# Performance work log

Hardware: AMD Instinct MI355X
Metric: run time of the kernel (lower is better)

## Reference

```python
import jax, jax.numpy as jnp
import numpy as np

HEADS = 16
DHEAD = 128
B, S, DMODEL = 2, 2048, 2048


def setup_inputs() -> dict:
    key = jax.random.key(0)
    k1, k2, k3 = jax.random.split(key, 3)
    x = jax.random.normal(k1, (B, S, DMODEL), dtype=jnp.float32)
    # Linear weights, stored as [in, out] so forward is x @ w (no bias).
    w_in = jax.random.normal(k2, (DMODEL, 3 * HEADS * DHEAD), dtype=jnp.float32) * (DMODEL ** -0.5)
    w_out = jax.random.normal(k3, (HEADS * DHEAD, DMODEL), dtype=jnp.float32) * ((HEADS * DHEAD) ** -0.5)
    # Causal mask: True = masked (strictly upper triangular), broadcast over batch & heads.
    mask = jnp.triu(jnp.ones((S, S), dtype=jnp.bool_), k=1)[None, None, :, :]
    return {"x": x, "w_in": w_in, "w_out": w_out, "mask": mask}


def reference(x, w_in, w_out, mask):
    b, s, _ = x.shape
    # Fused QKV projection: [b,s,3*H*dh] -> [b,s,H,3*dh] -> chunk into q,k,v [b,s,H,dh]
    projected = (x @ w_in).reshape(b, s, HEADS, 3 * DHEAD)
    q, k, v = jnp.split(projected, 3, axis=-1)
    # Scores [b,H,l,L], scaled by 1/sqrt(dhead)
    scale = 1.0 / (DHEAD ** 0.5)
    a = jnp.einsum("blhd,bLhd->bhlL", q, k) * scale
    a = jnp.where(mask, -jnp.inf, a)
    a = jax.nn.softmax(a, axis=-1)
    # Weighted values -> [b,l,H,dh] -> flatten heads -> output projection
    out = jnp.einsum("bhlL,bLhd->blhd", a, v).reshape(b, s, HEADS * DHEAD)
    return out @ w_out
```

## Files before the change

### kernel.cpp

```cpp
#include <hip/hip_runtime.h>

#define HD    16
#define DH    128
#define BB    2
#define SS    2048
#define DM    2048
#define NQKV  6144
#define MTOT  4096

typedef short   bfx8  __attribute__((ext_vector_type(8)));
typedef float   f32x4 __attribute__((ext_vector_type(4)));

__device__ __forceinline__ unsigned short f2bf(float f) {
  union { float f; unsigned int u; } c; c.f = f;
  unsigned int u = c.u + 0x7FFFu + ((c.u >> 16) & 1u);
  return (unsigned short)(u >> 16);
}

__device__ __forceinline__ void gload_lds16(const unsigned short* g, unsigned short* l) {
  __builtin_amdgcn_global_load_lds(
      (const __attribute__((address_space(1))) unsigned int*)g,
      (__attribute__((address_space(3))) unsigned int*)l, 16, 0, 0);
}

#define BARS() do { asm volatile("s_waitcnt lgkmcnt(0)" ::: "memory");               \
                    __builtin_amdgcn_sched_barrier(0); __builtin_amdgcn_s_barrier(); \
                    __builtin_amdgcn_sched_barrier(0); } while (0)
#define VMCNT10() do { asm volatile("s_waitcnt vmcnt(10)" ::: "memory"); \
                       __builtin_amdgcn_sched_barrier(0); } while (0)
#define VMCNT6() do { asm volatile("s_waitcnt vmcnt(6)" ::: "memory"); \
                      __builtin_amdgcn_sched_barrier(0); } while (0)

__global__ __launch_bounds__(256) void prep_fused_k(const float* __restrict__ x,
                                                    unsigned short* __restrict__ Xb,
                                                    const float* __restrict__ w_in,
                                                    unsigned short* __restrict__ Wit) {
  __shared__ float t[32][33];
  const int bid = (int)blockIdx.x;
  if (bid < 8192) {
    const int i = bid * 256 + (int)threadIdx.x;
    const float4 v = *(const float4*)(x + (size_t)i * 4);
    ushort4 o;
    o.x = f2bf(v.x); o.y = f2bf(v.y); o.z = f2bf(v.z); o.w = f2bf(v.w);
    *(ushort4*)(Xb + (size_t)i * 4) = o;
    return;
  }
  const int tb = bid - 8192;
  const int c0 = (tb % 192) * 32, r0 = (tb / 192) * 32;
  const int tx = threadIdx.x & 31, ty = threadIdx.x >> 5;
#pragma unroll
  for (int i = 0; i < 4; i++) {
    int r = r0 + ty + i * 8;
    t[ty + i * 8][tx] = w_in[(size_t)r * NQKV + c0 + tx];
  }
  __syncthreads();
#pragma unroll
  for (int i = 0; i < 4; i++) {
    int c = c0 + ty + i * 8;
    Wit[(size_t)c * DM + r0 + tx] = f2bf(t[tx][ty + i * 8]);
  }
}

__global__ __launch_bounds__(256, 2) void gemm128_qkv_k(const unsigned short* __restrict__ A,
                                                        const unsigned short* __restrict__ Bt,
                                                        unsigned short* __restrict__ Qg,
                                                        unsigned short* __restrict__ Kg,
                                                        unsigned short* __restrict__ Vg,
                                                        int K) {
  __shared__ __align__(16) unsigned short Asb[2][128 * 64];
  __shared__ __align__(16) unsigned short Bsb[2][192 * 64];
  const int tid = threadIdx.x;
  const int lane = tid & 63, wid = tid >> 6;
  const int wr = wid >> 1, wc = wid & 1;
  const int cbase = lane & 15, rgrp = lane >> 4;
  const int bid = (int)blockIdx.x;
  const int id = (bid & 7) * 128 + (bid >> 3);
  const int nb = id >> 5, mb = id & 31;
  const size_t m0 = (size_t)mb * 128, n0 = (size_t)nb * 192;
  const int nkt = K >> 6;

#define STAGE_A32(u_, g_) do {                                                          \
    const int uc_ = ((u_) < nkt ? (u_) : (nkt - 1));                                    \
    const int r_ = tid >> 3, s_ = tid & 7;                                              \
    gload_lds16(A + (m0 + (g_) * 32 + r_) * (size_t)K + uc_ * 64 +                      \
                    (((s_ * 16) ^ ((r_ & 7) << 4)) >> 1),                               \
                &Asb[(u_) & 1][(g_) * 2048] + tid * 8); } while (0)
#define STAGE_B32(u_, g_) do {                                                          \
    const int uc_ = ((u_) < nkt ? (u_) : (nkt - 1));                                    \
    const int r_ = tid >> 3, s_ = tid & 7;                                              \
    gload_lds16(Bt + (n0 + (g_) * 32 + r_) * (size_t)K + uc_ * 64 +                     \
                    (((s_ * 16) ^ ((r_ & 7) << 4)) >> 1),                               \
                &Bsb[(u_) & 1][(g_) * 2048] + tid * 8); } while (0)

  const int axor = (cbase & 7) << 4;
  int a_off[2], b_off[2];
#pragma unroll
  for (int ks = 0; ks < 2; ks++) {
    a_off[ks] = ((wr * 64 + cbase) * 128 + ((ks * 64 + rgrp * 16) ^ axor)) >> 1;
    b_off[ks] = ((wc * 96 + cbase) * 128 + ((ks * 64 + rgrp * 16) ^ axor)) >> 1;
  }

#define RD_AALL(dst_, p_) do { _Pragma("unroll")                                         \
    for (int mf_ = 0; mf_ < 4; mf_++) { _Pragma("unroll")                                \
      for (int ks_ = 0; ks_ < 2; ks_++)                                                  \
        dst_[mf_][ks_] = *(const bfx8*)((p_) + a_off[ks_] + mf_ * 1024); } } while (0)
#define RD_BP(dst_, p_, P_) do { _Pragma("unroll")                                       \
    for (int nf_ = 0; nf_ < 2; nf_++) { _Pragma("unroll")                                \
      for (int ks_ = 0; ks_ < 2; ks_++)                                                  \
        dst_[nf_][ks_] = *(const bfx8*)((p_) + b_off[ks_] + (nf_ + (P_)) * 1024); } } while (0)

#define MFMA_P(no_, AF_, BF_) do {                                                       \
    __builtin_amdgcn_s_setprio(1);                                                      \
    _Pragma("unroll")                                                                    \
    for (int mf_ = 0; mf_ < 4; mf_++) { _Pragma("unroll")                                \
      for (int nf_ = 0; nf_ < 2; nf_++) { _Pragma("unroll")                              \
        for (int ks_ = 0; ks_ < 2; ks_++)                                                \
          acc[mf_][nf_ + (no_)] = __builtin_amdgcn_mfma_f32_16x16x32_bf16(               \
              AF_[mf_][ks_], BF_[nf_][ks_], acc[mf_][nf_ + (no_)], 0, 0, 0); } }         \
    __builtin_amdgcn_s_setprio(0); } while (0)

  f32x4 acc[4][6];
  const f32x4 z = {0.f, 0.f, 0.f, 0.f};
#pragma unroll
  for (int mf = 0; mf < 4; mf++)
#pragma unroll
    for (int nf = 0; nf < 6; nf++) acc[mf][nf] = z;

  STAGE_A32(0, 0); STAGE_A32(0, 1); STAGE_A32(0, 2); STAGE_A32(0, 3);
  STAGE_B32(0, 0); STAGE_B32(0, 1); STAGE_B32(0, 2);
  STAGE_B32(0, 3); STAGE_B32(0, 4); STAGE_B32(0, 5);
  STAGE_A32(1, 0); STAGE_A32(1, 1); STAGE_A32(1, 2); STAGE_A32(1, 3);
  STAGE_B32(1, 0); STAGE_B32(1, 1); STAGE_B32(1, 2);
  STAGE_B32(1, 3); STAGE_B32(1, 4); STAGE_B32(1, 5);
  VMCNT10();
  BARS();
  bfx8 aA[4][2], b01A[2][2], aB[4][2], b01B[2][2];
  RD_AALL(aA, &Asb[0][0]);
  RD_BP(b01A, &Bsb[0][0], 0);
  BARS();

#define TILE_BODY(u_, Ac, B01c, An, B01n) do {                                           \
    const unsigned short* Bs_  = &Bsb[(u_) & 1][0];                                      \
    const unsigned short* Asn_ = &Asb[((u_) + 1) & 1][0];                                \
    const unsigned short* Bsn_ = &Bsb[((u_) + 1) & 1][0];                                \
    bfx8 b23[2][2], b45[2][2];                                                           \
        \
                                                             \
    RD_BP(b23, Bs_, 2);                                                                  \
    STAGE_A32((u_) + 2, 0); STAGE_A32((u_) + 2, 1);                                      \
    STAGE_A32((u_) + 2, 2); STAGE_A32((u_) + 2, 3);                                      \
    STAGE_B32((u_) + 2, 0); STAGE_B32((u_) + 2, 3);                                      \
    BARS();                                                                              \
    MFMA_P(0, Ac, B01c);                                                                 \
         \
    RD_BP(b45, Bs_, 4);                                                                  \
    STAGE_B32((u_) + 2, 1); STAGE_B32((u_) + 2, 4);                                      \
    BARS();                                                                              \
    MFMA_P(2, Ac, b23);                                                                  \
        \
                                           \
    STAGE_B32((u_) + 2, 2); STAGE_B32((u_) + 2, 5);                                      \
    VMCNT10();                                                                           \
    BARS();                                                                              \
    RD_AALL(An, Asn_);                                                                   \
    RD_BP(B01n, Bsn_, 0);                                                                \
    MFMA_P(4, Ac, b45);                                                                  \
    BARS();                                                                              \
  } while (0)

#pragma unroll 1
  for (int u = 0; u < nkt; u += 2) {
    TILE_BODY(u,     aA, b01A, aB, b01B);
    TILE_BODY(u + 1, aB, b01B, aA, b01A);
  }
#undef TILE_BODY
#undef STAGE_A32
#undef STAGE_B32

#pragma unroll
  for (int mf = 0; mf < 4; mf++)
#pragma unroll
    for (int nf = 0; nf < 6; nf++) {
      const int nn = (int)n0 + wc * 96 + nf * 16;
      const int h = nn / 384, tt = (nn >> 7) % 3;
      const int d = (nn & 127) + cbase;
      const int row0 = (int)m0 + wr * 64 + mf * 16 + rgrp * 4;
      const int bb = row0 >> 11;
      const int s0 = row0 & 2047;
      if (tt == 2) {
        ushort4 v;
        v.x = f2bf(acc[mf][nf][0]); v.y = f2bf(acc[mf][nf][1]);
        v.z = f2bf(acc[mf][nf][2]); v.w = f2bf(acc[mf][nf][3]);
        *(ushort4*)(Vg + ((size_t)(bb * HD + h) * DH + d) * SS + s0) = v;
      } else {
        unsigned short* dst = (tt == 0 ? Qg : Kg);
#pragma unroll
        for (int r = 0; r < 4; r++)
          dst[((size_t)(bb * HD + h) * SS + s0 + r) * DH + d] = f2bf(acc[mf][nf][r]);
      }
    }
}

__global__ __launch_bounds__(512, 2) void gemm256_out_k(const unsigned short* __restrict__ A,
                                                        const unsigned short* __restrict__ Bt,
                                                        float* __restrict__ C, int K, int ldc) {
  __shared__ __align__(16) unsigned short Asb[2][256 * 64];
  __shared__ __align__(16) unsigned short Bsb[2][128 * 64];
  const int tid = threadIdx.x;
  const int lane = tid & 63, wid = tid >> 6;
  const int wr = wid >> 2, wc = wid & 3;
  const int cbase = lane & 15, rgrp = lane >> 4;
  const int bid = (int)blockIdx.x;
  const int id = (bid & 7) * 32 + (bid >> 3);
  const int nb = id >> 4, mb = id & 15;
  const size_t m0 = (size_t)mb * 256, n0 = (size_t)nb * 128;
  const int nkt = K >> 6;

#define STAGE_AO(u_, g_) do {                                                           \
    const int uc_ = ((u_) < nkt ? (u_) : (nkt - 1));                                    \
    const int r_ = tid >> 3, s_ = tid & 7;                                              \
    gload_lds16(A + (m0 + (g_) * 64 + r_) * (size_t)K + uc_ * 64 +                      \
                    (((s_ * 16) ^ ((r_ & 7) << 4)) >> 1),                               \
                &Asb[(u_) & 1][(g_) * 4096] + tid * 8); } while (0)
#define STAGE_BO(u_, g_) do {                                                           \
    const int uc_ = ((u_) < nkt ? (u_) : (nkt - 1));                                    \
    const int r_ = tid >> 3, s_ = tid & 7;                                              \
    gload_lds16(Bt + (n0 + (g_) * 64 + r_) * (size_t)K + uc_ * 64 +                     \
                    (((s_ * 16) ^ ((r_ & 7) << 4)) >> 1),                               \
                &Bsb[(u_) & 1][(g_) * 4096] + tid * 8); } while (0)

  const int axor = (cbase & 7) << 4;
  int a_off[2], b_off[2];
#pragma unroll
  for (int ks = 0; ks < 2; ks++) {
    a_off[ks] = ((wr * 128 + cbase) * 128 + ((ks * 64 + rgrp * 16) ^ axor)) >> 1;
    b_off[ks] = ((wc * 32 + cbase) * 128 + ((ks * 64 + rgrp * 16) ^ axor)) >> 1;
  }

#define RD_A03(dst_, p_) do { _Pragma("unroll")                                          \
    for (int mf_ = 0; mf_ < 4; mf_++) { _Pragma("unroll")                                \
      for (int ks_ = 0; ks_ < 2; ks_++)                                                  \
        dst_[mf_][ks_] = *(const bfx8*)((p_) + a_off[ks_] + mf_ * 1024); } } while (0)
#define RD_A47(dst_, p_) do { _Pragma("unroll")                                          \
    for (int mf_ = 0; mf_ < 4; mf_++) { _Pragma("unroll")                                \
      for (int ks_ = 0; ks_ < 2; ks_++)                                                  \
        dst_[mf_][ks_] = *(const bfx8*)((p_) + a_off[ks_] + (mf_ + 4) * 1024); } } while (0)
#define RD_B01(dst_, p_) do { _Pragma("unroll")                                          \
    for (int nf_ = 0; nf_ < 2; nf_++) { _Pragma("unroll")                                \
      for (int ks_ = 0; ks_ < 2; ks_++)                                                  \
        dst_[nf_][ks_] = *(const bfx8*)((p_) + b_off[ks_] + nf_ * 1024); } } while (0)

#define MFMA_O(mo_, AF_, BF_) do {                                                       \
    __builtin_amdgcn_s_setprio(1);                                                      \
    _Pragma("unroll")                                                                    \
    for (int mf_ = 0; mf_ < 4; mf_++) { _Pragma("unroll")                                \
      for (int nf_ = 0; nf_ < 2; nf_++) { _Pragma("unroll")                              \
        for (int ks_ = 0; ks_ < 2; ks_++)                                                \
          acc[mf_ + (mo_)][nf_] = __builtin_amdgcn_mfma_f32_16x16x32_bf16(               \
              AF_[mf_][ks_], BF_[nf_][ks_], acc[mf_ + (mo_)][nf_], 0, 0, 0); } }         \
    __builtin_amdgcn_s_setprio(0); } while (0)

  f32x4 acc[8][2];
  const f32x4 z = {0.f, 0.f, 0.f, 0.f};
#pragma unroll
  for (int mf = 0; mf < 8; mf++)
#pragma unroll
    for (int nf = 0; nf < 2; nf++) acc[mf][nf] = z;

  STAGE_AO(0, 0); STAGE_AO(0, 1); STAGE_AO(0, 2); STAGE_AO(0, 3);
  STAGE_BO(0, 0); STAGE_BO(0, 1);
  STAGE_AO(1, 0); STAGE_AO(1, 1); STAGE_AO(1, 2); STAGE_AO(1, 3);
  STAGE_BO(1, 0); STAGE_BO(1, 1);
  VMCNT6();
  BARS();
  bfx8 a03A[4][2], b01A[2][2], a03B[4][2], b01B[2][2];
  RD_A03(a03A, &Asb[0][0]);
  RD_B01(b01A, &Bsb[0][0]);
  BARS();

#define TILE_BODY_O(u_, A03c, B01c, A03n, B01n) do {                                     \
    const unsigned short* As_  = &Asb[(u_) & 1][0];                                      \
    const unsigned short* Asn_ = &Asb[((u_) + 1) & 1][0];                                \
    const unsigned short* Bsn_ = &Bsb[((u_) + 1) & 1][0];                                \
    bfx8 a47[4][2];                                                                      \
    RD_A47(a47, As_);                                                                    \
    STAGE_AO((u_) + 2, 0); STAGE_AO((u_) + 2, 2);                                        \
    BARS();                                                                              \
    MFMA_O(0, A03c, B01c);                                                               \
    STAGE_AO((u_) + 2, 1); STAGE_AO((u_) + 2, 3);                                        \
    STAGE_BO((u_) + 2, 0); STAGE_BO((u_) + 2, 1);                                        \
    VMCNT6();                                                                            \
    BARS();                                                                              \
    RD_A03(A03n, Asn_);                                                                  \
    RD_B01(B01n, Bsn_);                                                                  \
    MFMA_O(4, a47, B01c);                                                                \
    BARS();                                                                              \
  } while (0)

#pragma unroll 1
  for (int u = 0; u < nkt; u += 2) {
    TILE_BODY_O(u,     a03A, b01A, a03B, b01B);
    TILE_BODY_O(u + 1, a03B, b01B, a03A, b01A);
  }
#undef TILE_BODY_O
#undef STAGE_AO
#undef STAGE_BO

#pragma unroll
  for (int mf = 0; mf < 8; mf++)
#pragma unroll
    for (int nf = 0; nf < 2; nf++)
#pragma unroll
      for (int r = 0; r < 4; r++) {
        size_t row = m0 + wr * 128 + mf * 16 + rgrp * 4 + r;
        size_t col = n0 + wc * 32 + nf * 16 + cbase;
        C[row * ldc + col] = acc[mf][nf][r];
      }
}

__global__ __launch_bounds__(256) void attn_wot_k(const unsigned short* __restrict__ Qg,
                                                  const unsigned short* __restrict__ Kg,
                                                  const unsigned short* __restrict__ Vg,
                                                  unsigned short* __restrict__ ao,
                                                  const float* __restrict__ w_out,
                                                  unsigned short* __restrict__ Wot) {
  __shared__ __align__(16) unsigned short Klds[2][64 * 128];
  __shared__ __align__(16) unsigned short Vt[2][128 * 64];
  __shared__ __align__(16) unsigned short Plds[4][16 * 64];
  const int tid = threadIdx.x;
  const int bid = (int)blockIdx.x;

  if (bid >= 1024) {
    float* t = (float*)&Klds[0][0];
    const int tb = bid - 1024;
    const int c0 = (tb & 63) * 32, r0 = (tb >> 6) * 32;
    const int tx = tid & 31, ty = tid >> 5;
#pragma unroll
    for (int i = 0; i < 4; i++) {
      int r = r0 + ty + i * 8;
      t[(ty + i * 8) * 33 + tx] = w_out[(size_t)r * DM + c0 + tx];
    }
    __syncthreads();
#pragma unroll
    for (int i = 0; i < 4; i++) {
      int c = c0 + ty + i * 8;
      Wot[(size_t)c * DM + r0 + tx] = f2bf(t[tx * 33 + ty + i * 8]);
    }
    return;
  }

  const int lane = tid & 63, wid = tid >> 6;
  const int cbase = lane & 15, rgrp = lane >> 4;
  const int cx = (cbase & 7) << 4;

  const int bh = (bid & 7) * 4 + ((bid >> 3) & 3);
  const int qt = 31 - (bid >> 5);
  const int b = bh >> 4, h = bh & 15;
  const int qbase = qt * 64;

  const unsigned short* qp0 = Qg + (size_t)(b * HD + h) * SS * DH;
  const unsigned short* kp  = Kg + (size_t)(b * HD + h) * SS * DH;
  const unsigned short* vp  = Vg + (size_t)(b * HD + h) * DH * SS;
  const float scale = 0.08838834764831845f;
  const f32x4 z = {0.f, 0.f, 0.f, 0.f};
  const int qi = qbase + wid * 16 + cbase;

  bfx8 qf[4];
  {
    const unsigned short* qp = qp0 + (size_t)qi * DH;
#pragma unroll
    for (int ks = 0; ks < 4; ks++) qf[ks] = *(const bfx8*)(qp + ks * 32 + rgrp * 8);
  }

  float m_run = -1e30f, l_run = 0.f;
  f32x4 o[8];
#pragma unroll
  for (int mb = 0; mb < 8; mb++) o[mb] = z;

#define STAGE_T(t_, s_) do {                                                        \
    const int kvb_ = (t_) * 64;                                                     \
    _Pragma("unroll")                                                               \
    for (int i_ = 0; i_ < 4; i_++) {                                                \
      int idx_ = i_ * 256 + tid;                                                    \
      int r_ = idx_ >> 4, bo_ = (idx_ & 15) * 16;                                   \
      gload_lds16(kp + (size_t)(kvb_ + r_) * DH + ((bo_ ^ ((r_ & 7) << 4)) >> 1),   \
                  &Klds[s_][idx_ * 8]);                                             \
    }                                                                               \
    _Pragma("unroll")                                                               \
    for (int i_ = 0; i_ < 4; i_++) {                                                \
      int idx_ = i_ * 256 + tid;                                                    \
      int d_ = idx_ >> 3, bo_ = (idx_ & 7) * 16;                                    \
      gload_lds16(vp + (size_t)d_ * SS + kvb_ + ((bo_ ^ ((d_ & 7) << 4)) >> 1),     \
                  &Vt[s_][idx_ * 8]);                                               \
    } } while (0)

  const int ntiles = qt + 1;
  STAGE_T(0, 0);
  __syncthreads();

  for (int t = 0; t < ntiles; ++t) {
    const int sel = t & 1;
    if (t + 1 < ntiles) STAGE_T(t + 1, sel ^ 1);
    const unsigned short* Ks_ = &Klds[sel][0];
    const unsigned short* Vs_ = &Vt[sel][0];
    const int kvb = t * 64;

    f32x4 s[4];
#pragma unroll
    for (int mf = 0; mf < 4; mf++) s[mf] = z;
#pragma unroll
    for (int mf = 0; mf < 4; mf++)
#pragma unroll
      for (int ks = 0; ks < 4; ks++) {
        bfx8 kf = *(const bfx8*)(Ks_ + (((mf * 16 + cbase) * 256 + ((ks * 64 + rgrp * 16) ^ cx)) >> 1));
        s[mf] = __builtin_amdgcn_mfma_f32_16x16x32_bf16(kf, qf[ks], s[mf], 0, 0, 0);
      }

    float sv[4][4];
    const bool diag = (t == ntiles - 1);
#pragma unroll
    for (int mf = 0; mf < 4; mf++)
#pragma unroll
      for (int r = 0; r < 4; r++) {
        float v = s[mf][r] * scale;
        if (diag && (kvb + mf * 16 + rgrp * 4 + r > qi)) v = -1e30f;
        sv[mf][r] = v;
      }
    float tm = sv[0][0];
#pragma unroll
    for (int mf = 0; mf < 4; mf++)
#pragma unroll
      for (int r = 0; r < 4; r++) tm = fmaxf(tm, sv[mf][r]);
    tm = fmaxf(tm, __shfl_xor(tm, 16));
    tm = fmaxf(tm, __shfl_xor(tm, 32));
    const float mnew = fmaxf(m_run, tm);
    float p[4][4];
    float rs = 0.f;
#pragma unroll
    for (int mf = 0; mf < 4; mf++)
#pragma unroll
      for (int r = 0; r < 4; r++) { p[mf][r] = __expf(sv[mf][r] - mnew); rs += p[mf][r]; }
    rs += __shfl_xor(rs, 16);
    rs += __shfl_xor(rs, 32);
    const float alpha = __expf(m_run - mnew);
    l_run = l_run * alpha + rs;
    m_run = mnew;
#pragma unroll
    for (int mb = 0; mb < 8; mb++)
#pragma unroll
      for (int r = 0; r < 4; r++) o[mb][r] *= alpha;

#pragma unroll
    for (int mf = 0; mf < 4; mf++)
#pragma unroll
      for (int rr = 0; rr < 2; rr++) {
        unsigned int pp = (unsigned int)f2bf(p[mf][2 * rr]) |
                          ((unsigned int)f2bf(p[mf][2 * rr + 1]) << 16);
        *(unsigned int*)((char*)&Plds[wid][0] +
                         (cbase * 128 + ((mf * 32 + rgrp * 8 + rr * 4) ^ cx))) = pp;
      }
    bfx8 pf[2];
#pragma unroll
    for (int k2 = 0; k2 < 2; k2++)
      pf[k2] = *(const bfx8*)((const char*)&Plds[wid][0] +
                              (cbase * 128 + ((k2 * 64 + rgrp * 16) ^ cx)));

#pragma unroll
    for (int mb = 0; mb < 8; mb++)
#pragma unroll
      for (int k2 = 0; k2 < 2; k2++) {
        bfx8 vf = *(const bfx8*)(Vs_ + (((mb * 16 + cbase) * 128 + ((k2 * 64 + rgrp * 16) ^ cx)) >> 1));
        o[mb] = __builtin_amdgcn_mfma_f32_16x16x32_bf16(vf, pf[k2], o[mb], 0, 0, 0);
      }
    __syncthreads();
  }
#undef STAGE_T

  const float rinv = 1.0f / l_run;
  unsigned short* aop = ao + ((size_t)(b * SS + qi)) * DM + h * DH + rgrp * 4;
#pragma unroll
  for (int mb = 0; mb < 8; mb++) {
    ushort4 v;
    v.x = f2bf(o[mb][0] * rinv); v.y = f2bf(o[mb][1] * rinv);
    v.z = f2bf(o[mb][2] * rinv); v.w = f2bf(o[mb][3] * rinv);
    *(ushort4*)(aop + mb * 16) = v;
  }
}

extern "C" void kernel_launch(void* const* d_in, const int* in_sizes, int n_in,
                              void* d_out, int out_size, void* d_ws, size_t ws_size,
                              hipStream_t stream) {
  (void)in_sizes; (void)n_in; (void)out_size; (void)ws_size;
  const float* x     = (const float*)d_in[0];
  const float* w_in  = (const float*)d_in[1];
  const float* w_out = (const float*)d_in[2];
  float* out = (float*)d_out;

  char* ws = (char*)d_ws;
  unsigned short* Xb  = (unsigned short*)(ws);
  unsigned short* Wit = (unsigned short*)(ws + (16ull << 20));
  unsigned short* Wot = (unsigned short*)(ws + (40ull << 20));
  unsigned short* Qg  = (unsigned short*)(ws + (48ull << 20));
  unsigned short* Kg  = (unsigned short*)(ws + (64ull << 20));
  unsigned short* Vg  = (unsigned short*)(ws + (80ull << 20));
  unsigned short* AO  = (unsigned short*)(ws + (96ull << 20));

  prep_fused_k<<<20480, 256, 0, stream>>>(x, Xb, w_in, Wit);
  gemm128_qkv_k<<<1024, 256, 0, stream>>>(Xb, Wit, Qg, Kg, Vg, DM);
  attn_wot_k<<<5120, 256, 0, stream>>>(Qg, Kg, Vg, AO, w_out, Wot);
  gemm256_out_k<<<256, 512, 0, stream>>>(AO, Wot, out, DM, DM);
}
```

Measured before the change: 229.8 us.

## Retile output projection GEMM to 128x128 tiles with 256-thread blocks

Replaces the 256x128 output-projection GEMM (512 threads, 256 blocks) with a 128x128 tile variant using 256 threads and 512 blocks. Each wave now computes a 64x64 sub-tile instead of 128x32, and staging is rewritten around 32-row load groups with a vmcnt(8) wait. The goal is more blocks for better CU occupancy and load balance on the 4096x2048 output. The cost is lower per-block data reuse and more total global traffic. It depends on RD_AALL, RD_BP and MFMA_P macros that are assumed to be defined elsewhere, likely in the QKV GEMM.

Result: no change. 230.1 us, median of 4 (+0.1%).

```diff
diff --git a/kernel.cpp b/kernel.cpp
--- a/kernel.cpp
+++ b/kernel.cpp
@@ -28,7 +28,7 @@
                     __builtin_amdgcn_sched_barrier(0); } while (0)
 #define VMCNT10() do { asm volatile("s_waitcnt vmcnt(10)" ::: "memory"); \
                        __builtin_amdgcn_sched_barrier(0); } while (0)
-#define VMCNT6() do { asm volatile("s_waitcnt vmcnt(6)" ::: "memory"); \
+#define VMCNT8() do { asm volatile("s_waitcnt vmcnt(8)" ::: "memory"); \
                       __builtin_amdgcn_sched_barrier(0); } while (0)
 
 __global__ __launch_bounds__(256) void prep_fused_k(const float* __restrict__ x,
@@ -201,119 +201,101 @@
     }
 }
 
-__global__ __launch_bounds__(512, 2) void gemm256_out_k(const unsigned short* __restrict__ A,
+__global__ __launch_bounds__(256, 2) void gemm128_out_k(const unsigned short* __restrict__ A,
                                                         const unsigned short* __restrict__ Bt,
                                                         float* __restrict__ C, int K, int ldc) {
-  __shared__ __align__(16) unsigned short Asb[2][256 * 64];
+  __shared__ __align__(16) unsigned short Asb[2][128 * 64];
   __shared__ __align__(16) unsigned short Bsb[2][128 * 64];
   const int tid = threadIdx.x;
   const int lane = tid & 63, wid = tid >> 6;
-  const int wr = wid >> 2, wc = wid & 3;
+  const int wr = wid >> 1, wc = wid & 1;
   const int cbase = lane & 15, rgrp = lane >> 4;
   const int bid = (int)blockIdx.x;
-  const int id = (bid & 7) * 32 + (bid >> 3);
-  const int nb = id >> 4, mb = id & 15;
-  const size_t m0 = (size_t)mb * 256, n0 = (size_t)nb * 128;
+  const int id = (bid & 7) * 64 + (bid >> 3);
+  const int nb = id >> 5, mb = id & 31;
+  const size_t m0 = (size_t)mb * 128, n0 = (size_t)nb * 128;
   const int nkt = K >> 6;
 
-#define STAGE_AO(u_, g_) do {                                                           \
+#define STAGE_AO32(u_, g_) do {                                                         \
     const int uc_ = ((u_) < nkt ? (u_) : (nkt - 1));                                    \
     const int r_ = tid >> 3, s_ = tid & 7;                                              \
-    gload_lds16(A + (m0 + (g_) * 64 + r_) * (size_t)K + uc_ * 64 +                      \
+    gload_lds16(A + (m0 + (g_) * 32 + r_) * (size_t)K + uc_ * 64 +                      \
                     (((s_ * 16) ^ ((r_ & 7) << 4)) >> 1),                               \
-                &Asb[(u_) & 1][(g_) * 4096] + tid * 8); } while (0)
-#define STAGE_BO(u_, g_) do {                                                           \
+                &Asb[(u_) & 1][(g_) * 2048] + tid * 8); } while (0)
+#define STAGE_BO32(u_, g_) do {                                                         \
     const int uc_ = ((u_) < nkt ? (u_) : (nkt - 1));                                    \
     const int r_ = tid >> 3, s_ = tid & 7;                                              \
-    gload_lds16(Bt + (n0 + (g_) * 64 + r_) * (size_t)K + uc_ * 64 +                     \
+    gload_lds16(Bt + (n0 + (g_) * 32 + r_) * (size_t)K + uc_ * 64 +                     \
                     (((s_ * 16) ^ ((r_ & 7) << 4)) >> 1),                               \
-                &Bsb[(u_) & 1][(g_) * 4096] + tid * 8); } while (0)
+                &Bsb[(u_) & 1][(g_) * 2048] + tid * 8); } while (0)
 
   const int axor = (cbase & 7) << 4;
   int a_off[2], b_off[2];
 #pragma unroll
   for (int ks = 0; ks < 2; ks++) {
-    a_off[ks] = ((wr * 128 + cbase) * 128 + ((ks * 64 + rgrp * 16) ^ axor)) >> 1;
-    b_off[ks] = ((wc * 32 + cbase) * 128 + ((ks * 64 + rgrp * 16) ^ axor)) >> 1;
-  }
-
-#define RD_A03(dst_, p_) do { _Pragma("unroll")                                          \
-    for (int mf_ = 0; mf_ < 4; mf_++) { _Pragma("unroll")                                \
-      for (int ks_ = 0; ks_ < 2; ks_++)                                                  \
-        dst_[mf_][ks_] = *(const bfx8*)((p_) + a_off[ks_] + mf_ * 1024); } } while (0)
-#define RD_A47(dst_, p_) do { _Pragma("unroll")                                          \
-    for (int mf_ = 0; mf_ < 4; mf_++) { _Pragma("unroll")                                \
-      for (int ks_ = 0; ks_ < 2; ks_++)                                                  \
-        dst_[mf_][ks_] = *(const bfx8*)((p_) + a_off[ks_] + (mf_ + 4) * 1024); } } while (0)
-#define RD_B01(dst_, p_) do { _Pragma("unroll")                                          \
-    for (int nf_ = 0; nf_ < 2; nf_++) { _Pragma("unroll")                                \
-      for (int ks_ = 0; ks_ < 2; ks_++)                                                  \
-        dst_[nf_][ks_] = *(const bfx8*)((p_) + b_off[ks_] + nf_ * 1024); } } while (0)
-
-#define MFMA_O(mo_, AF_, BF_) do {                                                       \
-    __builtin_amdgcn_s_setprio(1);                                                      \
-    _Pragma("unroll")                                                                    \
-    for (int mf_ = 0; mf_ < 4; mf_++) { _Pragma("unroll")                                \
-      for (int nf_ = 0; nf_ < 2; nf_++) { _Pragma("unroll")                              \
-        for (int ks_ = 0; ks_ < 2; ks_++)                                                \
-          acc[mf_ + (mo_)][nf_] = __builtin_amdgcn_mfma_f32_16x16x32_bf16(               \
-              AF_[mf_][ks_], BF_[nf_][ks_], acc[mf_ + (mo_)][nf_], 0, 0, 0); } }         \
-    __builtin_amdgcn_s_setprio(0); } while (0)
-
-  f32x4 acc[8][2];
+    a_off[ks] = ((wr * 64 + cbase) * 128 + ((ks * 64 + rgrp * 16) ^ axor)) >> 1;
+    b_off[ks] = ((wc * 64 + cbase) * 128 + ((ks * 64 + rgrp * 16) ^ axor)) >> 1;
+  }
+
+  f32x4 acc[4][4];
   const f32x4 z = {0.f, 0.f, 0.f, 0.f};
 #pragma unroll
-  for (int mf = 0; mf < 8; mf++)
-#pragma unroll
-    for (int nf = 0; nf < 2; nf++) acc[mf][nf] = z;
-
-  STAGE_AO(0, 0); STAGE_AO(0, 1); STAGE_AO(0, 2); STAGE_AO(0, 3);
-  STAGE_BO(0, 0); STAGE_BO(0, 1);
-  STAGE_AO(1, 0); STAGE_AO(1, 1); STAGE_AO(1, 2); STAGE_AO(1, 3);
-  STAGE_BO(1, 0); STAGE_BO(1, 1);
-  VMCNT6();
+  for (int mf = 0; mf < 4; mf++)
+#pragma unroll
+    for (int nf = 0; nf < 4; nf++) acc[mf][nf] = z;
+
+  STAGE_AO32(0, 0); STAGE_AO32(0, 1); STAGE_AO32(0, 2); STAGE_AO32(0, 3);
+  STAGE_BO32(0, 0); STAGE_BO32(0, 1); STAGE_BO32(0, 2); STAGE_BO32(0, 3);
+  STAGE_AO32(1, 0); STAGE_AO32(1, 1); STAGE_AO32(1, 2); STAGE_AO32(1, 3);
+  STAGE_BO32(1, 0); STAGE_BO32(1, 1); STAGE_BO32(1, 2); STAGE_BO32(1, 3);
+  VMCNT8();
   BARS();
-  bfx8 a03A[4][2], b01A[2][2], a03B[4][2], b01B[2][2];
-  RD_A03(a03A, &Asb[0][0]);
-  RD_B01(b01A, &Bsb[0][0]);
+  bfx8 aA[4][2], b01A[2][2], aB[4][2], b01B[2][2];
+  RD_AALL(aA, &Asb[0][0]);
+  RD_BP(b01A, &Bsb[0][0], 0);
   BARS();
 
-#define TILE_BODY_O(u_, A03c, B01c, A03n, B01n) do {                                     \
-    const unsigned short* As_  = &Asb[(u_) & 1][0];                                      \
+#define TILE_BODY_Q(u_, Ac, B01c, An, B01n) do {                                         \
+    const unsigned short* Bs_  = &Bsb[(u_) & 1][0];                                      \
     const unsigned short* Asn_ = &Asb[((u_) + 1) & 1][0];                                \
     const unsigned short* Bsn_ = &Bsb[((u_) + 1) & 1][0];                                \
-    bfx8 a47[4][2];                                                                      \
-    RD_A47(a47, As_);                                                                    \
-    STAGE_AO((u_) + 2, 0); STAGE_AO((u_) + 2, 2);                                        \
-    BARS();                                                                              \
-    MFMA_O(0, A03c, B01c);                                                               \
-    STAGE_AO((u_) + 2, 1); STAGE_AO((u_) + 2, 3);                                        \
-    STAGE_BO((u_) + 2, 0); STAGE_BO((u_) + 2, 1);                                        \
-    VMCNT6();                                                                            \
-    BARS();                                                                              \
-    RD_A03(A03n, Asn_);                                                                  \
-    RD_B01(B01n, Bsn_);                                                                  \
-    MFMA_O(4, a47, B01c);                                                                \
+    bfx8 b23[2][2];                                                                      \
+        \
+                                                             \
+    RD_BP(b23, Bs_, 2);                                                                  \
+    STAGE_AO32((u_) + 2, 0); STAGE_AO32((u_) + 2, 1);                                    \
+    STAGE_AO32((u_) + 2, 2); STAGE_AO32((u_) + 2, 3);                                    \
+    STAGE_BO32((u_) + 2, 0); STAGE_BO32((u_) + 2, 2);                                    \
+    BARS();                                                                              \
+    MFMA_P(0, Ac, B01c);                                                                 \
+         \
+                             \
+    STAGE_BO32((u_) + 2, 1); STAGE_BO32((u_) + 2, 3);                                    \
+    VMCNT8();                                                                            \
+    BARS();                                                                              \
+    RD_AALL(An, Asn_);                                                                   \
+    RD_BP(B01n, Bsn_, 0);                                                                \
+    MFMA_P(2, Ac, b23);                                                                  \
     BARS();                                                                              \
   } while (0)
 
 #pragma unroll 1
   for (int u = 0; u < nkt; u += 2) {
-    TILE_BODY_O(u,     a03A, b01A, a03B, b01B);
-    TILE_BODY_O(u + 1, a03B, b01B, a03A, b01A);
-  }
-#undef TILE_BODY_O
-#undef STAGE_AO
-#undef STAGE_BO
-
-#pragma unroll
-  for (int mf = 0; mf < 8; mf++)
-#pragma unroll
-    for (int nf = 0; nf < 2; nf++)
+    TILE_BODY_Q(u,     aA, b01A, aB, b01B);
+    TILE_BODY_Q(u + 1, aB, b01B, aA, b01A);
+  }
+#undef TILE_BODY_Q
+#undef STAGE_AO32
+#undef STAGE_BO32
+
+#pragma unroll
+  for (int mf = 0; mf < 4; mf++)
+#pragma unroll
+    for (int nf = 0; nf < 4; nf++)
 #pragma unroll
       for (int r = 0; r < 4; r++) {
-        size_t row = m0 + wr * 128 + mf * 16 + rgrp * 4 + r;
-        size_t col = n0 + wc * 32 + nf * 16 + cbase;
+        size_t row = m0 + wr * 64 + mf * 16 + rgrp * 4 + r;
+        size_t col = n0 + wc * 64 + nf * 16 + cbase;
         C[row * ldc + col] = acc[mf][nf][r];
       }
 }
@@ -508,5 +490,5 @@
   prep_fused_k<<<20480, 256, 0, stream>>>(x, Xb, w_in, Wit);
   gemm128_qkv_k<<<1024, 256, 0, stream>>>(Xb, Wit, Qg, Kg, Vg, DM);
   attn_wot_k<<<5120, 256, 0, stream>>>(Qg, Kg, Vg, AO, w_out, Wot);
-  gemm256_out_k<<<256, 512, 0, stream>>>(AO, Wot, out, DM, DM);
-}
+  gemm128_out_k<<<512, 256, 0, stream>>>(AO, Wot, out, DM, DM);
+}
```
